# Kernel optimization log

Measured on AMD Instinct MI355X. Metric: run time of the kernel, lower is better.

## Reference

```python
import jax, jax.numpy as jnp
import numpy as np

N, E, B = 200000, 800000, 16
NODE_FEAT = 140  # last col = shape element type id
N_OPS, N_TYPES = 120, 8
OP_EMB, TYPE_EMB, CFG = 32, 4, 18
H = 64
CAT = (NODE_FEAT - 1) + TYPE_EMB + OP_EMB + CFG  # 193


def _lin(k, i, o):
    s = 1.0 / np.sqrt(i)
    return jax.random.uniform(k, (i, o), jnp.float32, -s, s)


def setup_inputs() -> dict:
    key = jax.random.key(0)
    ks = jax.random.split(key, 20)
    nf = jax.random.normal(ks[0], (N, NODE_FEAT - 1), jnp.float32)
    ty = jax.random.randint(ks[1], (N, 1), 0, N_TYPES).astype(jnp.float32)
    inp = {
        "node_feat": jnp.concatenate([nf, ty], axis=1),
        "node_config_feat": jax.random.normal(ks[2], (N, CFG), jnp.float32),
        "node_opcode": jax.random.randint(ks[3], (N,), 0, N_OPS),
        "edge_index": jax.random.randint(ks[4], (2, E), 0, N),
        "batch": jnp.sort(jax.random.randint(ks[5], (N,), 0, B)),
        "op_emb": jax.random.normal(ks[6], (N_OPS, OP_EMB), jnp.float32),
        "type_emb": jax.random.normal(ks[7], (N_TYPES, TYPE_EMB), jnp.float32),
        "lin_w": _lin(ks[8], CAT, 2 * H),
        "lin_b": jnp.zeros((2 * H,), jnp.float32),
        "post_w": _lin(ks[9], H, 1),
        "post_b": jnp.zeros((1,), jnp.float32),
    }
    kk = 10
    for l, ind in enumerate([2 * H, H, H]):
        inp[f"p{l}_wp"] = _lin(ks[kk], ind, ind); kk += 1  # SAGE project lin
        inp[f"p{l}_bp"] = jnp.zeros((ind,), jnp.float32)
        inp[f"p{l}_wl"] = _lin(ks[kk], ind, H); kk += 1    # lin_l (on aggregated)
        inp[f"p{l}_bl"] = jnp.zeros((H,), jnp.float32)
        inp[f"p{l}_wr"] = _lin(ks[kk], ind, H); kk += 1    # lin_r (root, no bias)
    return inp


def _sage(x, src, dst, deg_inv, wp, bp, wl, bl, wr):
    # PyG SAGEConv(project=True, normalize=True), mean aggregation
    xp = jax.nn.relu(x @ wp + bp)
    agg = jax.ops.segment_sum(xp[src], dst, num_segments=x.shape[0]) * deg_inv
    out = agg @ wl + bl + x @ wr
    n = jnp.linalg.norm(out, axis=-1, keepdims=True)
    return out / jnp.maximum(n, 1e-12)


def reference(node_feat, node_config_feat, node_opcode, edge_index, batch,
              op_emb, type_emb, lin_w, lin_b, post_w, post_b,
              p0_wp, p0_bp, p0_wl, p0_bl, p0_wr,
              p1_wp, p1_bp, p1_wl, p1_bl, p1_wr,
              p2_wp, p2_bp, p2_wl, p2_bl, p2_wr):
    lps = [(p0_wp, p0_bp, p0_wl, p0_bl, p0_wr),
           (p1_wp, p1_bp, p1_wl, p1_bl, p1_wr),
           (p2_wp, p2_bp, p2_wl, p2_bl, p2_wr)]
    ty = jnp.take(type_emb, node_feat[:, -1].astype(jnp.int32), axis=0)
    op = jnp.take(op_emb, node_opcode, axis=0)
    x = jnp.concatenate([node_feat[:, :-1], ty, op, node_config_feat], axis=-1)
    x = jax.nn.relu(x @ lin_w + lin_b)  # (N, 128)
    src, dst = edge_index[0], edge_index[1]
    deg = jax.ops.segment_sum(jnp.ones((E,), x.dtype), dst, num_segments=N)
    deg_inv = (1.0 / jnp.maximum(deg, 1.0))[:, None]
    for (wp, bp, wl, bl, wr) in lps:
        x = _sage(x, src, dst, deg_inv, wp, bp, wl, bl, wr)
    # global max + mean pool per graph
    gmax = jax.ops.segment_max(x, batch, num_segments=B)
    gsum = jax.ops.segment_sum(x, batch, num_segments=B)
    cnt = jax.ops.segment_sum(jnp.ones((N,), x.dtype), batch, num_segments=B)
    g = gmax + gsum / jnp.maximum(cnt, 1.0)[:, None]
    g = g / jnp.linalg.norm(g, axis=-1, keepdims=True)
    return g @ post_w + post_b  # (B, 1); eval path returns x_graph
```

## Files before the change

### kernel.cpp

```cpp
#include <hip/hip_runtime.h>

typedef _Float16 half8 __attribute__((ext_vector_type(8)));
typedef _Float16 h4 __attribute__((ext_vector_type(4)));
typedef float f32x4 __attribute__((ext_vector_type(4)));

__device__ __forceinline__ unsigned fkey(float f) {
  unsigned u = __float_as_uint(f);
  return (u & 0x80000000u) ? ~u : (u | 0x80000000u);
}
__device__ __forceinline__ float funkey(unsigned k) {
  unsigned u = (k & 0x80000000u) ? (k ^ 0x80000000u) : ~k;
  return __uint_as_float(u);
}

struct WD { const float* src; _Float16* dst; int K, NC, Kpad, base; };
struct WDs { WD d[10]; int total; };

__global__ __launch_bounds__(256) void k_wconv(WDs w) {
  int idx = blockIdx.x * 256 + threadIdx.x;
  if (idx >= w.total) return;
#pragma unroll
  for (int i = 0; i < 10; ++i) {
    int rel = idx - w.d[i].base;
    int sz = w.d[i].NC * w.d[i].Kpad;
    if (rel >= 0 && rel < sz) {
      int n = rel / w.d[i].Kpad;
      int k = rel - n * w.d[i].Kpad;
      w.d[i].dst[rel] = (k < w.d[i].K) ? (_Float16)w.d[i].src[(size_t)k * w.d[i].NC + n]
                                       : (_Float16)0.f;
      return;
    }
  }
}

__global__ __launch_bounds__(256) void k_count(const int* __restrict__ dst,
                                               int* __restrict__ counts, int E) {
  int e = blockIdx.x * 256 + threadIdx.x;
  if (e < E) atomicAdd(&counts[dst[e]], 1);
}

__global__ __launch_bounds__(256) void k_scan1(const int* __restrict__ counts,
                                               int* __restrict__ offsets,
                                               int* __restrict__ blockSums, int N) {
  __shared__ int sm[256];
  int tid = threadIdx.x;
  int gid = blockIdx.x * 256 + tid;
  int v = (gid < N) ? counts[gid] : 0;
  sm[tid] = v;
  __syncthreads();
  for (int off = 1; off < 256; off <<= 1) {
    int t = (tid >= off) ? sm[tid - off] : 0;
    __syncthreads();
    sm[tid] += t;
    __syncthreads();
  }
  if (gid < N) offsets[gid] = sm[tid] - v;
  if (tid == 255) blockSums[blockIdx.x] = sm[255];
}

__global__ __launch_bounds__(1024) void k_scan2(int* __restrict__ blockSums, int NB) {
  __shared__ int sm[1024];
  int tid = threadIdx.x;
  int v = (tid < NB) ? blockSums[tid] : 0;
  sm[tid] = v;
  __syncthreads();
  for (int off = 1; off < 1024; off <<= 1) {
    int t = (tid >= off) ? sm[tid - off] : 0;
    __syncthreads();
    sm[tid] += t;
    __syncthreads();
  }
  if (tid < NB) blockSums[tid] = sm[tid] - v;
}

__global__ __launch_bounds__(256) void k_scan3(const int* __restrict__ counts,
                                               int* __restrict__ offsets,
                                               const int* __restrict__ blockSums,
                                               int* __restrict__ fillpos,
                                               float* __restrict__ deginv, int N, int E) {
  int gid = blockIdx.x * 256 + threadIdx.x;
  if (gid < N) {
    int off = offsets[gid] + blockSums[gid >> 8];
    offsets[gid] = off;
    fillpos[gid] = off;
    deginv[gid] = 1.f / fmaxf((float)counts[gid], 1.f);
  }
  if (gid == 0) offsets[N] = E;
}

__global__ __launch_bounds__(256) void k_fill(const int* __restrict__ src,
                                              const int* __restrict__ dst,
                                              int* __restrict__ fillpos,
                                              int* __restrict__ esrc, int E) {
  int e = blockIdx.x * 256 + threadIdx.x;
  if (e < E) {
    int p = atomicAdd(&fillpos[dst[e]], 1);
    esrc[p] = src[e];
  }
}

__global__ __launch_bounds__(256) void k_feat(const float* __restrict__ node_feat,
                                              const float* __restrict__ cfgf,
                                              const int* __restrict__ opcode,
                                              const float* __restrict__ op_emb,
                                              const float* __restrict__ type_emb,
                                              _Float16* __restrict__ Out, int N) {
  __shared__ _Float16 sF[64 * 144];
  __shared__ _Float16 sC[64 * 18];
  __shared__ int sOp[64];
  const int base = blockIdx.x * 64;
  const int nrem = min(64, N - base);

  {
    const float4* g = (const float4*)(node_feat + (size_t)base * 140);
    const int tot4 = nrem * 35;
    for (int i = threadIdx.x; i < tot4; i += 256) {
      float4 v = g[i];
      int r = i / 35, c4 = i - r * 35;
      h4 o;
      o[0] = (_Float16)v.x; o[1] = (_Float16)v.y;
      o[2] = (_Float16)v.z; o[3] = (_Float16)v.w;
      *(h4*)(sF + r * 144 + c4 * 4) = o;
    }
  }
  {
    const float* g = cfgf + (size_t)base * 18;
    const int tot = nrem * 18;
    for (int i = threadIdx.x; i < tot; i += 256) sC[i] = (_Float16)g[i];
  }
  if (threadIdx.x < 64)
    sOp[threadIdx.x] = (base + threadIdx.x < N) ? opcode[base + threadIdx.x] : 0;
  __syncthreads();

#pragma unroll
  for (int it = 0; it < 7; ++it) {
    int chunk = it * 256 + threadIdx.x;
    int r = chunk / 28;
    int c0 = (chunk - r * 28) * 8;
    if (r >= nrem) continue;
    const _Float16* fr = sF + r * 144;
    half8 o;
    if (c0 <= 128) {
      o = *(const half8*)(fr + c0);
    } else if (c0 == 136) {
      o[0] = fr[136]; o[1] = fr[137]; o[2] = fr[138];
      int ty = min(max((int)(float)fr[139], 0), 7);
      const float* te = type_emb + ty * 4;
      o[3] = (_Float16)te[0]; o[4] = (_Float16)te[1];
      o[5] = (_Float16)te[2]; o[6] = (_Float16)te[3];
      o[7] = (_Float16)op_emb[sOp[r] * 32 + 0];
    } else if (c0 < 168) {
      const float* op = op_emb + sOp[r] * 32 + (c0 - 143);
#pragma unroll
      for (int j = 0; j < 8; ++j) o[j] = (_Float16)op[j];
    } else if (c0 == 168) {
      const float* op = op_emb + sOp[r] * 32;
#pragma unroll
      for (int j = 0; j < 7; ++j) o[j] = (_Float16)op[25 + j];
      o[7] = sC[r * 18 + 0];
    } else if (c0 < 192) {
      const _Float16* c = sC + r * 18 + (c0 - 175);
#pragma unroll
      for (int j = 0; j < 8; ++j) o[j] = c[j];
    } else if (c0 == 192) {
      o = half8{};
      o[0] = sC[r * 18 + 17];
    } else {
      o = half8{};
    }
    *(half8*)(Out + (size_t)(base + r) * 224 + c0) = o;
  }
}

template <int K0, int K1, int NC, int MODE>
__global__ __launch_bounds__(256) void k_mm(
    const _Float16* __restrict__ A0, const _Float16* __restrict__ W0,
    const _Float16* __restrict__ A1, const _Float16* __restrict__ W1,
    const float* __restrict__ bias, _Float16* __restrict__ Out, int N) {
  constexpr int NT = NC / 16;
  constexpr int RT = 4;
  constexpr int KP0 = K0 + 8;
  constexpr int KP1 = K1 + 8;
  __shared__ _Float16 sB0[NC * KP0];
  __shared__ _Float16 sB1[(K1 > 0) ? (NC * KP1) : 8];

  for (int idx = threadIdx.x; idx < NC * (K0 / 8); idx += 256) {
    int nn = idx / (K0 / 8), k8 = idx - nn * (K0 / 8);
    *(half8*)(sB0 + nn * KP0 + k8 * 8) = *(const half8*)(W0 + (size_t)nn * K0 + k8 * 8);
  }
  if constexpr (K1 > 0) {
    for (int idx = threadIdx.x; idx < NC * (K1 / 8); idx += 256) {
      int nn = idx / (K1 / 8), k8 = idx - nn * (K1 / 8);
      *(half8*)(sB1 + nn * KP1 + k8 * 8) = *(const half8*)(W1 + (size_t)nn * K1 + k8 * 8);
    }
  }
  __syncthreads();

  const int lane = threadIdx.x & 63, wave = threadIdx.x >> 6;
  const int quad = lane >> 4, l15 = lane & 15;
  const int r0 = blockIdx.x * 256 + wave * 64;

  f32x4 acc[RT][NT];
#pragma unroll
  for (int rt = 0; rt < RT; ++rt)
#pragma unroll
    for (int t = 0; t < NT; ++t) acc[rt][t] = (f32x4)0.f;

  {
    const _Float16* ap = A0 + (size_t)(r0 + l15) * K0 + quad * 8;
#pragma unroll
    for (int k = 0; k < K0; k += 32) {
      half8 a[RT];
#pragma unroll
      for (int rt = 0; rt < RT; ++rt) a[rt] = *(const half8*)(ap + (size_t)rt * 16 * K0 + k);
#pragma unroll
      for (int t = 0; t < NT; ++t) {
        half8 b = *(const half8*)(sB0 + (t * 16 + l15) * KP0 + quad * 8 + k);
#pragma unroll
        for (int rt = 0; rt < RT; ++rt)
          acc[rt][t] = __builtin_amdgcn_mfma_f32_16x16x32_f16(a[rt], b, acc[rt][t], 0, 0, 0);
      }
    }
  }
  if constexpr (K1 > 0) {
    const _Float16* ap = A1 + (size_t)(r0 + l15) * K1 + quad * 8;
#pragma unroll
    for (int k = 0; k < K1; k += 32) {
      half8 a[RT];
#pragma unroll
      for (int rt = 0; rt < RT; ++rt) a[rt] = *(const half8*)(ap + (size_t)rt * 16 * K1 + k);
#pragma unroll
      for (int t = 0; t < NT; ++t) {
        half8 b = *(const half8*)(sB1 + (t * 16 + l15) * KP1 + quad * 8 + k);
#pragma unroll
        for (int rt = 0; rt < RT; ++rt)
          acc[rt][t] = __builtin_amdgcn_mfma_f32_16x16x32_f16(a[rt], b, acc[rt][t], 0, 0, 0);
      }
    }
  }

#pragma unroll
  for (int rt = 0; rt < RT; ++rt) {
#pragma unroll
    for (int t = 0; t < NT; ++t) {
      float bv = bias[t * 16 + l15];
      acc[rt][t][0] += bv; acc[rt][t][1] += bv;
      acc[rt][t][2] += bv; acc[rt][t][3] += bv;
    }
    if constexpr (MODE == 1) {
      f32x4 ss = (f32x4)0.f;
#pragma unroll
      for (int t = 0; t < NT; ++t) ss += acc[rt][t] * acc[rt][t];
#pragma unroll
      for (int j = 0; j < 4; ++j) {
        float s = ss[j];
        s += __shfl_xor(s, 1);
        s += __shfl_xor(s, 2);
        s += __shfl_xor(s, 4);
        s += __shfl_xor(s, 8);
        float sc = 1.f / fmaxf(sqrtf(s), 1e-12f);
#pragma unroll
        for (int t = 0; t < NT; ++t) acc[rt][t][j] *= sc;
      }
    } else {
#pragma unroll
      for (int t = 0; t < NT; ++t) {
        acc[rt][t][0] = fmaxf(acc[rt][t][0], 0.f);
        acc[rt][t][1] = fmaxf(acc[rt][t][1], 0.f);
        acc[rt][t][2] = fmaxf(acc[rt][t][2], 0.f);
        acc[rt][t][3] = fmaxf(acc[rt][t][3], 0.f);
      }
    }
#pragma unroll
    for (int j = 0; j < 4; ++j) {
      int r = r0 + rt * 16 + quad * 4 + j;
      if (r < N) {
#pragma unroll
        for (int t = 0; t < NT; ++t)
          Out[(size_t)r * NC + t * 16 + l15] = (_Float16)acc[rt][t][j];
      }
    }
  }
}

template <int NC>
__global__ __launch_bounds__(256) void k_agg(const _Float16* __restrict__ xp,
                                             const int* __restrict__ offs,
                                             const int* __restrict__ esrc,
                                             const float* __restrict__ deginv,
                                             _Float16* __restrict__ agg, int N) {
  constexpr int LPN = NC / 4;
  int t = blockIdx.x * 256 + threadIdx.x;
  int node = t / LPN;
  int lane = t - node * LPN;
  if (node >= N) return;
  int s0 = offs[node], s1 = offs[node + 1];
  double a0 = 0., a1 = 0., a2 = 0., a3 = 0.;
  for (int i = s0; i < s1; i += 4) {
    int nlast = s1 - 1;
    int e0 = esrc[i];
    int e1 = esrc[min(i + 1, nlast)];
    int e2 = esrc[min(i + 2, nlast)];
    int e3 = esrc[min(i + 3, nlast)];
    h4 v0 = ((const h4*)(xp + (size_t)e0 * NC))[lane];
    h4 v1 = ((const h4*)(xp + (size_t)e1 * NC))[lane];
    h4 v2 = ((const h4*)(xp + (size_t)e2 * NC))[lane];
    h4 v3 = ((const h4*)(xp + (size_t)e3 * NC))[lane];
    a0 += (double)(float)v0[0]; a1 += (double)(float)v0[1];
    a2 += (double)(float)v0[2]; a3 += (double)(float)v0[3];
    if (i + 1 < s1) { a0 += (double)(float)v1[0]; a1 += (double)(float)v1[1];
                      a2 += (double)(float)v1[2]; a3 += (double)(float)v1[3]; }
    if (i + 2 < s1) { a0 += (double)(float)v2[0]; a1 += (double)(float)v2[1];
                      a2 += (double)(float)v2[2]; a3 += (double)(float)v2[3]; }
    if (i + 3 < s1) { a0 += (double)(float)v3[0]; a1 += (double)(float)v3[1];
                      a2 += (double)(float)v3[2]; a3 += (double)(float)v3[3]; }
  }
  double di = (double)deginv[node];
  h4 o;
  o[0] = (_Float16)(a0 * di); o[1] = (_Float16)(a1 * di);
  o[2] = (_Float16)(a2 * di); o[3] = (_Float16)(a3 * di);
  ((h4*)(agg + (size_t)node * NC))[lane] = o;
}

__global__ __launch_bounds__(256) void k_pool1(const _Float16* __restrict__ x,
                                               const int* __restrict__ batch,
                                               unsigned* __restrict__ gkey,
                                               double* __restrict__ gsum,
                                               int* __restrict__ gcnt, int N) {
  int chunk = blockIdx.x * 4 + (threadIdx.x >> 6);
  int lane = threadIdx.x & 63;
  int n0 = chunk * 64;
  if (n0 >= N) return;
  int n1 = min(n0 + 64, N);
  float rmax = -3.4e38f;
  double rsum = 0.;
  int rcnt = 0, curb = batch[n0];
  for (int n = n0; n < n1; ++n) {
    int b = batch[n];
    if (b != curb) {
      atomicMax(&gkey[curb * 64 + lane], fkey(rmax));
      atomicAdd(&gsum[curb * 64 + lane], rsum);
      if (lane == 0) atomicAdd(&gcnt[curb], rcnt);
      rmax = -3.4e38f; rsum = 0.; rcnt = 0; curb = b;
    }
    float v = (float)x[(size_t)n * 64 + lane];
    rmax = fmaxf(rmax, v);
    rsum += (double)v;
    rcnt++;
  }
  atomicMax(&gkey[curb * 64 + lane], fkey(rmax));
  atomicAdd(&gsum[curb * 64 + lane], rsum);
  if (lane == 0) atomicAdd(&gcnt[curb], rcnt);
}

__global__ __launch_bounds__(1024) void k_pool2(const unsigned* __restrict__ gkey,
                                                const double* __restrict__ gsum,
                                                const int* __restrict__ gcnt,
                                                const float* __restrict__ post_w,
                                                const float* __restrict__ post_b,
                                                float* __restrict__ out) {
  int b = threadIdx.x >> 6, lane = threadIdx.x & 63;
  float m = funkey(gkey[b * 64 + lane]);
  double s = gsum[b * 64 + lane];
  double c = (double)gcnt[b];
  float g = m + (float)(s / fmax(c, 1.0));
  float ss = g * g;
#pragma unroll
  for (int off = 1; off < 64; off <<= 1) ss += __shfl_xor(ss, off);
  float gn = g / fmaxf(sqrtf(ss), 1e-30f);
  float contrib = gn * post_w[lane];
#pragma unroll
  for (int off = 1; off < 64; off <<= 1) contrib += __shfl_xor(contrib, off);
  if (lane == 0) out[b] = contrib + post_b[0];
}

extern "C" void kernel_launch(void* const* d_in, const int* in_sizes, int n_in,
                              void* d_out, int out_size, void* d_ws, size_t ws_size,
                              hipStream_t stream) {
  const float* node_feat = (const float*)d_in[0];
  const float* cfgf      = (const float*)d_in[1];
  const int*   opcode    = (const int*)d_in[2];
  const int*   eidx      = (const int*)d_in[3];
  const int*   batch     = (const int*)d_in[4];
  const float* op_emb    = (const float*)d_in[5];
  const float* type_emb  = (const float*)d_in[6];
  const float* lin_w     = (const float*)d_in[7];
  const float* lin_b     = (const float*)d_in[8];
  const float* post_w    = (const float*)d_in[9];
  const float* post_b    = (const float*)d_in[10];
  const float* wp[3] = {(const float*)d_in[11], (const float*)d_in[16], (const float*)d_in[21]};
  const float* bp[3] = {(const float*)d_in[12], (const float*)d_in[17], (const float*)d_in[22]};
  const float* wl[3] = {(const float*)d_in[13], (const float*)d_in[18], (const float*)d_in[23]};
  const float* bl[3] = {(const float*)d_in[14], (const float*)d_in[19], (const float*)d_in[24]};
  const float* wr[3] = {(const float*)d_in[15], (const float*)d_in[20], (const float*)d_in[25]};

  const int N = in_sizes[2];
  const int E = in_sizes[3] / 2;
  const int NPAD = ((N + 255) / 256) * 256;
  const int* e_src = eidx;
  const int* e_dst = eidx + E;

  char* p = (char*)d_ws;
  auto alloc = [&](size_t bytes) -> void* {
    void* r = (void*)p;
    p += (bytes + 255) & ~(size_t)255;
    return r;
  };
  _Float16* F  = (_Float16*)alloc((size_t)NPAD * 224 * 2);
  _Float16* X1 = (_Float16*)alloc((size_t)NPAD * 128 * 2);
  _Float16* R2 = (_Float16*)alloc((size_t)NPAD * 128 * 2);
  _Float16* R3 = (_Float16*)alloc((size_t)NPAD * 128 * 2);
  _Float16* WT = (_Float16*)alloc(86016 * 2);
  int* counts    = (int*)alloc((size_t)N * 4);
  int* offsets   = (int*)alloc((size_t)(N + 1) * 4);
  int* fillpos   = (int*)alloc((size_t)N * 4);
  float* deginv  = (float*)alloc((size_t)N * 4);
  int* blockSums = (int*)alloc(1024 * 4);
  int* esrc      = (int*)alloc((size_t)E * 4);
  unsigned* gkey = (unsigned*)alloc(16 * 64 * 4);
  double* gsum   = (double*)alloc(16 * 64 * 8);
  int* gcnt      = (int*)alloc(16 * 4);
  (void)ws_size; (void)n_in; (void)out_size;

  _Float16* WTenc = WT + 0;
  _Float16* WTp0  = WT + 28672;
  _Float16* WTl0  = WT + 45056;
  _Float16* WTr0  = WT + 53248;
  _Float16* WTp1  = WT + 61440;
  _Float16* WTl1  = WT + 65536;
  _Float16* WTr1  = WT + 69632;
  _Float16* WTp2  = WT + 73728;
  _Float16* WTl2  = WT + 77824;
  _Float16* WTr2  = WT + 81920;

  WDs wds;
  wds.d[0] = {lin_w, WTenc, 193, 128, 224, 0};
  wds.d[1] = {wp[0], WTp0, 128, 128, 128, 28672};
  wds.d[2] = {wl[0], WTl0, 128, 64, 128, 45056};
  wds.d[3] = {wr[0], WTr0, 128, 64, 128, 53248};
  wds.d[4] = {wp[1], WTp1, 64, 64, 64, 61440};
  wds.d[5] = {wl[1], WTl1, 64, 64, 64, 65536};
  wds.d[6] = {wr[1], WTr1, 64, 64, 64, 69632};
  wds.d[7] = {wp[2], WTp2, 64, 64, 64, 73728};
  wds.d[8] = {wl[2], WTl2, 64, 64, 64, 77824};
  wds.d[9] = {wr[2], WTr2, 64, 64, 64, 81920};
  wds.total = 86016;

  hipMemsetAsync(counts, 0, (size_t)N * 4, stream);
  hipMemsetAsync(gkey, 0, 16 * 64 * 4, stream);
  hipMemsetAsync(gsum, 0, 16 * 64 * 8, stream);
  hipMemsetAsync(gcnt, 0, 16 * 4, stream);

  const int nbE = (E + 255) / 256;
  const int nbN = (N + 255) / 256;
  const int nbMM = NPAD / 256;
  const int nbA128 = ((size_t)N * 32 + 255) / 256;
  const int nbA64  = ((size_t)N * 16 + 255) / 256;
  const int nbP = ((N + 63) / 64 + 3) / 4;

  k_wconv<<<(86016 + 255) / 256, 256, 0, stream>>>(wds);
  k_count<<<nbE, 256, 0, stream>>>(e_dst, counts, E);
  k_scan1<<<nbN, 256, 0, stream>>>(counts, offsets, blockSums, N);
  k_scan2<<<1, 1024, 0, stream>>>(blockSums, nbN);
  k_scan3<<<nbN, 256, 0, stream>>>(counts, offsets, blockSums, fillpos, deginv, N, E);
  k_fill<<<nbE, 256, 0, stream>>>(e_src, e_dst, fillpos, esrc, E);

  k_feat<<<(N + 63) / 64, 256, 0, stream>>>(node_feat, cfgf, opcode, op_emb, type_emb, F, N);
  k_mm<224, 0, 128, 0><<<nbMM, 256, 0, stream>>>(F, WTenc, nullptr, nullptr, lin_b, X1, N);

  k_mm<128, 0, 128, 0><<<nbMM, 256, 0, stream>>>(X1, WTp0, nullptr, nullptr, bp[0], R2, N);
  k_agg<128><<<nbA128, 256, 0, stream>>>(R2, offsets, esrc, deginv, R3, N);
  k_mm<128, 128, 64, 1><<<nbMM, 256, 0, stream>>>(R3, WTl0, X1, WTr0, bl[0], R2, N);
  k_mm<64, 0, 64, 0><<<nbMM, 256, 0, stream>>>(R2, WTp1, nullptr, nullptr, bp[1], R3, N);
  k_agg<64><<<nbA64, 256, 0, stream>>>(R3, offsets, esrc, deginv, X1, N);
  k_mm<64, 64, 64, 1><<<nbMM, 256, 0, stream>>>(X1, WTl1, R2, WTr1, bl[1], R3, N);
  k_mm<64, 0, 64, 0><<<nbMM, 256, 0, stream>>>(R3, WTp2, nullptr, nullptr, bp[2], X1, N);
  k_agg<64><<<nbA64, 256, 0, stream>>>(X1, offsets, esrc, deginv, R2, N);
  k_mm<64, 64, 64, 1><<<nbMM, 256, 0, stream>>>(R2, WTl2, R3, WTr2, bl[2], X1, N);

  k_pool1<<<nbP, 256, 0, stream>>>(X1, batch, gkey, gsum, gcnt, N);
  k_pool2<<<1, 1024, 0, stream>>>(gkey, gsum, gcnt, post_w, post_b, (float*)d_out);
}
```

Baseline: 723.4 us.

## Fuse feature assembly into encoder matmul, dropping the intermediate feature buffer

Replaces the separate feature-building kernel and the 224-wide encoder GEMM with one kernel. It assembles the concatenated fp16 row tile in shared memory and runs MFMA directly on it, reading weights from global memory. This removes the write and re-read of the N×224 fp16 intermediate buffer and one kernel launch. In exchange, B operands now come from global or L2 instead of LDS, and stores are scalar fp16 per element.

```diff
diff --git a/kernel.cpp b/kernel.cpp
--- a/kernel.cpp
+++ b/kernel.cpp
@@ -99,76 +99,108 @@
   }
 }
 
-__global__ __launch_bounds__(256) void k_feat(const float* __restrict__ node_feat,
-                                              const float* __restrict__ cfgf,
-                                              const int* __restrict__ opcode,
-                                              const float* __restrict__ op_emb,
-                                              const float* __restrict__ type_emb,
-                                              _Float16* __restrict__ Out, int N) {
-  __shared__ _Float16 sF[64 * 144];
-  __shared__ _Float16 sC[64 * 18];
-  __shared__ int sOp[64];
-  const int base = blockIdx.x * 64;
-  const int nrem = min(64, N - base);
-
-  {
-    const float4* g = (const float4*)(node_feat + (size_t)base * 140);
-    const int tot4 = nrem * 35;
-    for (int i = threadIdx.x; i < tot4; i += 256) {
-      float4 v = g[i];
-      int r = i / 35, c4 = i - r * 35;
-      h4 o;
+__global__ __launch_bounds__(256) void k_featenc(
+    const float* __restrict__ node_feat, const float* __restrict__ cfgf,
+    const int* __restrict__ opcode, const float* __restrict__ op_emb,
+    const float* __restrict__ type_emb, const _Float16* __restrict__ Wt,
+    const float* __restrict__ bias, _Float16* __restrict__ Out, int N) {
+  constexpr int K = 224, KP = 232, NC = 128, NT = 8;
+  __shared__ _Float16 sA[128 * KP];
+  const int base = blockIdx.x * 128;
+  const int nrem = min(128, N - base);
+
+  for (int i = threadIdx.x; i < 128 * 35; i += 256) {
+    int r = i / 35, k4 = i - r * 35;
+    h4 o = {};
+    if (r < nrem) {
+      float4 v = ((const float4*)(node_feat + (size_t)(base + r) * 140))[k4];
       o[0] = (_Float16)v.x; o[1] = (_Float16)v.y;
       o[2] = (_Float16)v.z; o[3] = (_Float16)v.w;
-      *(h4*)(sF + r * 144 + c4 * 4) = o;
-    }
-  }
+    }
+    *(h4*)(sA + r * KP + k4 * 4) = o;
+  }
+  for (int i = threadIdx.x; i < 128 * 25; i += 256) {
+    int r = i / 25, c = i - r * 25;
+    _Float16 v = (_Float16)0.f;
+    if (r < nrem && c < 18) v = (_Float16)cfgf[(size_t)(base + r) * 18 + c];
+    sA[r * KP + 175 + c] = v;
+  }
+  for (int i = threadIdx.x; i < 128 * 4; i += 256) {
+    int r = i >> 2, c = i & 3;
+    *(half8*)(sA + r * KP + 200 + c * 8) = half8{};
+  }
+  __syncthreads();
   {
-    const float* g = cfgf + (size_t)base * 18;
-    const int tot = nrem * 18;
-    for (int i = threadIdx.x; i < tot; i += 256) sC[i] = (_Float16)g[i];
-  }
-  if (threadIdx.x < 64)
-    sOp[threadIdx.x] = (base + threadIdx.x < N) ? opcode[base + threadIdx.x] : 0;
+    int r = threadIdx.x >> 1, hf = threadIdx.x & 1;
+    if (hf == 0) {
+      if (r < nrem) {
+        int n = base + r;
+        int ty = min(max((int)node_feat[(size_t)n * 140 + 139], 0), 7);
+        const float* te = type_emb + ty * 4;
+#pragma unroll
+        for (int j = 0; j < 4; ++j) sA[r * KP + 139 + j] = (_Float16)te[j];
+        const float* oe = op_emb + opcode[n] * 32;
+#pragma unroll
+        for (int j = 0; j < 16; ++j) sA[r * KP + 143 + j] = (_Float16)oe[j];
+      } else {
+#pragma unroll
+        for (int j = 0; j < 4; ++j) sA[r * KP + 139 + j] = (_Float16)0.f;
+#pragma unroll
+        for (int j = 0; j < 16; ++j) sA[r * KP + 143 + j] = (_Float16)0.f;
+      }
+    } else {
+      if (r < nrem) {
+        const float* oe = op_emb + opcode[base + r] * 32;
+#pragma unroll
+        for (int j = 16; j < 32; ++j) sA[r * KP + 143 + j] = (_Float16)oe[j];
+      } else {
+#pragma unroll
+        for (int j = 16; j < 32; ++j) sA[r * KP + 143 + j] = (_Float16)0.f;
+      }
+    }
+  }
   __syncthreads();
 
-#pragma unroll
-  for (int it = 0; it < 7; ++it) {
-    int chunk = it * 256 + threadIdx.x;
-    int r = chunk / 28;
-    int c0 = (chunk - r * 28) * 8;
-    if (r >= nrem) continue;
-    const _Float16* fr = sF + r * 144;
-    half8 o;
-    if (c0 <= 128) {
-      o = *(const half8*)(fr + c0);
-    } else if (c0 == 136) {
-      o[0] = fr[136]; o[1] = fr[137]; o[2] = fr[138];
-      int ty = min(max((int)(float)fr[139], 0), 7);
-      const float* te = type_emb + ty * 4;
-      o[3] = (_Float16)te[0]; o[4] = (_Float16)te[1];
-      o[5] = (_Float16)te[2]; o[6] = (_Float16)te[3];
-      o[7] = (_Float16)op_emb[sOp[r] * 32 + 0];
-    } else if (c0 < 168) {
-      const float* op = op_emb + sOp[r] * 32 + (c0 - 143);
-#pragma unroll
-      for (int j = 0; j < 8; ++j) o[j] = (_Float16)op[j];
-    } else if (c0 == 168) {
-      const float* op = op_emb + sOp[r] * 32;
-#pragma unroll
-      for (int j = 0; j < 7; ++j) o[j] = (_Float16)op[25 + j];
-      o[7] = sC[r * 18 + 0];
-    } else if (c0 < 192) {
-      const _Float16* c = sC + r * 18 + (c0 - 175);
-#pragma unroll
-      for (int j = 0; j < 8; ++j) o[j] = c[j];
-    } else if (c0 == 192) {
-      o = half8{};
-      o[0] = sC[r * 18 + 17];
-    } else {
-      o = half8{};
-    }
-    *(half8*)(Out + (size_t)(base + r) * 224 + c0) = o;
+  const int lane = threadIdx.x & 63, wave = threadIdx.x >> 6;
+  const int quad = lane >> 4, l15 = lane & 15;
+  const int rw = wave * 32;
+
+  f32x4 acc[2][NT];
+#pragma unroll
+  for (int rt = 0; rt < 2; ++rt)
+#pragma unroll
+    for (int t = 0; t < NT; ++t) acc[rt][t] = (f32x4)0.f;
+
+  const _Float16* ar = sA + (rw + l15) * KP + quad * 8;
+#pragma unroll
+  for (int k = 0; k < K; k += 32) {
+    half8 a0 = *(const half8*)(ar + k);
+    half8 a1 = *(const half8*)(ar + 16 * KP + k);
+#pragma unroll
+    for (int t = 0; t < NT; ++t) {
+      half8 b = *(const half8*)(Wt + (size_t)(t * 16 + l15) * K + quad * 8 + k);
+      acc[0][t] = __builtin_amdgcn_mfma_f32_16x16x32_f16(a0, b, acc[0][t], 0, 0, 0);
+      acc[1][t] = __builtin_amdgcn_mfma_f32_16x16x32_f16(a1, b, acc[1][t], 0, 0, 0);
+    }
+  }
+
+#pragma unroll
+  for (int rt = 0; rt < 2; ++rt) {
+#pragma unroll
+    for (int t = 0; t < NT; ++t) {
+      float bv = bias[t * 16 + l15];
+#pragma unroll
+      for (int j = 0; j < 4; ++j) acc[rt][t][j] = fmaxf(acc[rt][t][j] + bv, 0.f);
+    }
+#pragma unroll
+    for (int j = 0; j < 4; ++j) {
+      int r = base + rw + rt * 16 + quad * 4 + j;
+      if (r < N) {
+#pragma unroll
+        for (int t = 0; t < NT; ++t)
+          Out[(size_t)r * NC + t * 16 + l15] = (_Float16)acc[rt][t][j];
+      }
+    }
   }
 }
 
@@ -406,7 +438,6 @@
     p += (bytes + 255) & ~(size_t)255;
     return r;
   };
-  _Float16* F  = (_Float16*)alloc((size_t)NPAD * 224 * 2);
   _Float16* X1 = (_Float16*)alloc((size_t)NPAD * 128 * 2);
   _Float16* R2 = (_Float16*)alloc((size_t)NPAD * 128 * 2);
   _Float16* R3 = (_Float16*)alloc((size_t)NPAD * 128 * 2);
@@ -465,8 +496,8 @@
   k_scan3<<<nbN, 256, 0, stream>>>(counts, offsets, blockSums, fillpos, deginv, N, E);
   k_fill<<<nbE, 256, 0, stream>>>(e_src, e_dst, fillpos, esrc, E);
 
-  k_feat<<<(N + 63) / 64, 256, 0, stream>>>(node_feat, cfgf, opcode, op_emb, type_emb, F, N);
-  k_mm<224, 0, 128, 0><<<nbMM, 256, 0, stream>>>(F, WTenc, nullptr, nullptr, lin_b, X1, N);
+  k_featenc<<<(N + 127) / 128, 256, 0, stream>>>(node_feat, cfgf, opcode, op_emb,
+                                                 type_emb, WTenc, lin_b, X1, N);
 
   k_mm<128, 0, 128, 0><<<nbMM, 256, 0, stream>>>(X1, WTp0, nullptr, nullptr, bp[0], R2, N);
   k_agg<128><<<nbA128, 256, 0, stream>>>(R2, offsets, esrc, deginv, R3, N);
```

After: 737.9 us. 1.02x slower.
